# Performance work log

Hardware: AMD Instinct MI355X
Metric: run time of the kernel (lower is better)

The kernel has to match this reference:

```python
import jax, jax.numpy as jnp
import numpy as np

B, S, H = 32, 8192, 512


def setup_inputs() -> dict:
    key = jax.random.key(0)
    k1, k2, k3, k4 = jax.random.split(key, 4)
    output = jax.random.normal(k1, (B, 1, H), dtype=jnp.float32)
    context = jax.random.normal(k2, (B, S, H), dtype=jnp.float32)
    split_index = jax.random.randint(k3, (B,), 1, S - 1)  # avoid all-masked softmax rows
    W = jax.random.normal(k4, (H, 4 * H), dtype=jnp.float32) * (1.0 / np.sqrt(4 * H))
    b = jnp.zeros((H,), dtype=jnp.float32)
    return {"output": output, "context": context, "split_index": split_index, "W": W, "b": b}


def reference(output, context, split_index, W, b):
    Bb, Ss, Hh = context.shape
    rows = jnp.arange(Bb)
    pos = jnp.arange(Ss)

    # attn = bmm(output, context^T).squeeze(1) -> [B, S]
    attn = jnp.einsum('bih,bsh->bis', output, context)[:, 0, :]
    # torch code uses attn.data (detached) for all softmax paths
    attn_d = jax.lax.stop_gradient(attn)

    # forward-side mask: positions i < split_index kept
    fmask = pos[None, :] < split_index[:, None]  # [B, S] bool
    f_logits = jnp.where(fmask, attn_d, -jnp.inf)
    f_attn = jax.nn.softmax(f_logits, axis=1)
    f_attn = f_attn.at[rows, split_index].set(0.0)  # explicit zero at split position
    a_mix = jnp.einsum('bs,bsh->bh', f_attn, context)[:, None, :]  # [B,1,H]

    # NOTE: original source has `b_attn = f_attn.view(...)` (bug), so b_mix == a_mix.
    # The b-side masked softmax is computed but dead; we replicate the realized math.
    b_mix = a_mix

    # det_att = context[b, split_index[b], :]
    det_att = context[rows, split_index][:, None, :]  # [B,1,H]

    combined = jnp.concatenate((a_mix, b_mix, det_att, output), axis=2)  # [B,1,4H]
    out = jnp.tanh(combined @ W.T + b)  # Linear(4H->H) + Tanh, [B,1,H]
    return out, attn
```

## Files before the change

kernel.cpp:

```cpp
#include <hip/hip_runtime.h>
#include <math.h>

#define BATCH 32
#define SEQ   8192
#define HID   512
#define STRIPES 32
#define RPB   (SEQ / STRIPES)
#define CR    8
#define NCHUNK (RPB / CR)

typedef float f4 __attribute__((ext_vector_type(4)));
typedef float f2 __attribute__((ext_vector_type(2)));

#define VMWAIT(N) do { asm volatile("s_waitcnt vmcnt(" #N ")" ::: "memory"); \
                       __builtin_amdgcn_sched_barrier(0); } while (0)
#define LGKMWAIT0 do { asm volatile("s_waitcnt lgkmcnt(0)" ::: "memory"); \
                       __builtin_amdgcn_sched_barrier(0); } while (0)

__device__ __forceinline__ void gload_lds(const float* g, float* l) {
  __builtin_amdgcn_global_load_lds(
      (const __attribute__((address_space(1))) void*)g,
      (__attribute__((address_space(3))) void*)l, 16, 0, 0);
}

__global__ __launch_bounds__(256, 4) void k_pass1(
    const float* __restrict__ outp, const float* __restrict__ ctx,
    const int* __restrict__ split, float* __restrict__ attn_out,
    float* __restrict__ pacc, float* __restrict__ pmd)
{
  __shared__ float lds[2][CR][HID];
  const int tid = threadIdx.x, lane = tid & 63, wave = tid >> 6;
  const int b = blockIdx.x >> 5;
  const int stripe = blockIdx.x & 31;
  const int sp = split[b];
  const int s_base = stripe * RPB;

  const float* ob = outp + b * HID + lane * 8;
  const f4 o0 = *(const f4*)ob;
  const f4 o1 = *(const f4*)(ob + 4);

  const float* cbase = ctx + ((size_t)b * SEQ + s_base) * HID;
  float* ao = attn_out + (size_t)b * SEQ + s_base;

#pragma unroll
  for (int i = 0; i < 4; ++i) {
    const int o = (wave * 4 + i) * 256;
    gload_lds(cbase + o + lane * 4, &lds[0][0][0] + o);
  }
#pragma unroll
  for (int i = 0; i < 4; ++i) {
    const int o = (wave * 4 + i) * 256;
    gload_lds(cbase + CR * HID + o + lane * 4, &lds[1][0][0] + o);
  }

  float m = -INFINITY, d = 0.f;
  f4 acc0 = {0.f, 0.f, 0.f, 0.f}, acc1 = {0.f, 0.f, 0.f, 0.f};

#pragma unroll 1
  for (int c = 0; c < NCHUNK; ++c) {
    if (c == 0)                 VMWAIT(4);
    else if (c == NCHUNK - 1)   VMWAIT(1);
    else                        VMWAIT(5);

    const int cur = c & 1;
    f4 c0[2], c1[2];
#pragma unroll
    for (int k = 0; k < 2; ++k) {
      const float* rp = &lds[cur][wave * 2 + k][lane * 8];
      c0[k] = *(const f4*)rp;
      c1[k] = *(const f4*)(rp + 4);
    }
    LGKMWAIT0;

    float a2[2];
#pragma unroll
    for (int k = 0; k < 2; ++k) {
      float v = o0[0]*c0[k][0] + o0[1]*c0[k][1] + o0[2]*c0[k][2] + o0[3]*c0[k][3]
              + o1[0]*c1[k][0] + o1[1]*c1[k][1] + o1[2]*c1[k][2] + o1[3]*c1[k][3];
#pragma unroll
      for (int off = 32; off >= 1; off >>= 1) v += __shfl_xor(v, off, 64);
      a2[k] = v;
    }
    if (lane == 0) {
      f2 st = {a2[0], a2[1]};
      *(f2*)(ao + c * CR + wave * 2) = st;
    }

    if (c + 2 < NCHUNK) {
      const float* src = cbase + (size_t)(c + 2) * CR * HID;
      float* dst = &lds[cur][0][0];
#pragma unroll
      for (int i = 0; i < 4; ++i) {
        const int o = (wave * 4 + i) * 256;
        gload_lds(src + o + lane * 4, dst + o);
      }
    }

#pragma unroll
    for (int k = 0; k < 2; ++k) {
      const int s = s_base + c * CR + wave * 2 + k;
      if (s < sp) {
        const float v  = a2[k];
        const float nm = fmaxf(m, v);
        const float sc = __expf(m - nm);
        const float w  = __expf(v - nm);
        d = d * sc + w;
        acc0 = acc0 * sc + w * c0[k];
        acc1 = acc1 * sc + w * c1[k];
        m = nm;
      }
    }
  }

  __syncthreads();
  float* lacc = &lds[0][0][0];
  float* lmd  = &lds[1][0][0];
  *(f4*)(lacc + wave * HID + lane * 8)     = acc0;
  *(f4*)(lacc + wave * HID + lane * 8 + 4) = acc1;
  if (lane == 0) { lmd[wave * 2] = m; lmd[wave * 2 + 1] = d; }
  __syncthreads();

  const float M = fmaxf(fmaxf(lmd[0], lmd[2]), fmaxf(lmd[4], lmd[6]));
  const size_t pb = (size_t)b * STRIPES + stripe;
  float* pa = pacc + pb * HID;
  if (M == -INFINITY) {
    pa[tid * 2] = 0.f; pa[tid * 2 + 1] = 0.f;
    if (tid == 0) { pmd[pb * 2] = -INFINITY; pmd[pb * 2 + 1] = 0.f; }
  } else {
    float e[4], Dl = 0.f;
#pragma unroll
    for (int wv = 0; wv < 4; ++wv) {
      const float mw = lmd[wv * 2];
      e[wv] = (mw == -INFINITY) ? 0.f : __expf(mw - M);
      Dl += e[wv] * lmd[wv * 2 + 1];
    }
    float s0 = 0.f, s1 = 0.f;
#pragma unroll
    for (int wv = 0; wv < 4; ++wv) {
      s0 += e[wv] * lacc[wv * HID + tid * 2];
      s1 += e[wv] * lacc[wv * HID + tid * 2 + 1];
    }
    pa[tid * 2] = s0; pa[tid * 2 + 1] = s1;
    if (tid == 0) { pmd[pb * 2] = M; pmd[pb * 2 + 1] = Dl; }
  }
}

__global__ __launch_bounds__(256) void k_final(
    const float* __restrict__ outp, const float* __restrict__ ctx,
    const int* __restrict__ split, const float* __restrict__ W,
    const float* __restrict__ bias, const float* __restrict__ pacc,
    const float* __restrict__ pmd, float* __restrict__ out0)
{
  const int b = blockIdx.x >> 3, q = blockIdx.x & 7;
  const int tid = threadIdx.x;
  __shared__ float comb[3 * HID + 8];
  float* amixp = comb;
  float* detp  = comb + HID + 4;
  float* oupp  = comb + 2 * HID + 8;

  float M = -INFINITY;
#pragma unroll
  for (int c = 0; c < STRIPES; ++c) M = fmaxf(M, pmd[(b * STRIPES + c) * 2]);
  float wgt[STRIPES], D = 0.f;
#pragma unroll
  for (int c = 0; c < STRIPES; ++c) {
    const float mw = pmd[(b * STRIPES + c) * 2];
    wgt[c] = (mw == -INFINITY) ? 0.f : __expf(mw - M);
    D += wgt[c] * pmd[(b * STRIPES + c) * 2 + 1];
  }
  const float invD = 1.f / D;
  const int sp = split[b];
#pragma unroll
  for (int col = tid; col < HID; col += 256) {
    float s = 0.f;
#pragma unroll
    for (int c = 0; c < STRIPES; ++c)
      s += wgt[c] * pacc[((size_t)(b * STRIPES + c)) * HID + col];
    amixp[col] = s * invD;
    detp[col]  = ctx[((size_t)b * SEQ + sp) * HID + col];
    oupp[col]  = outp[b * HID + col];
  }
  __syncthreads();

  const int hl = tid >> 2, part = tid & 3;
  const int h = q * 64 + hl;
  const float* wr = W + (size_t)h * (4 * HID) + part * HID;
  const float* src = (part == 2) ? detp : (part == 3 ? oupp : amixp);
  float acc = 0.f;
#pragma unroll 4
  for (int k0 = 0; k0 < HID; k0 += 4) {
    const f4 w = *(const f4*)(wr + k0);
    const f4 x = *(const f4*)(src + k0);
    acc += w[0]*x[0] + w[1]*x[1] + w[2]*x[2] + w[3]*x[3];
  }
  acc += __shfl_xor(acc, 1, 64);
  acc += __shfl_xor(acc, 2, 64);
  if (part == 0) out0[b * HID + h] = tanhf(acc + bias[h]);
}

extern "C" void kernel_launch(void* const* d_in, const int* in_sizes, int n_in,
                              void* d_out, int out_size, void* d_ws, size_t ws_size,
                              hipStream_t stream)
{
  const float* outp = (const float*)d_in[0];
  const float* ctx  = (const float*)d_in[1];
  const int*   spl  = (const int*)d_in[2];
  const float* W    = (const float*)d_in[3];
  const float* bias = (const float*)d_in[4];

  float* out0   = (float*)d_out;
  float* attn_o = out0 + (size_t)BATCH * HID;

  float* pacc = (float*)d_ws;
  float* pmd  = pacc + (size_t)BATCH * STRIPES * HID;

  k_pass1<<<BATCH * STRIPES, 256, 0, stream>>>(outp, ctx, spl, attn_o, pacc, pmd);
  k_final<<<BATCH * 8,       256, 0, stream>>>(outp, ctx, spl, W, bias, pacc, pmd, out0);
}
```

Before: 126.0 us.

## Replace LDS double-buffered context staging with register prefetch pipeline per wave

Drops the global_load_lds double buffer with its manual waitcnt scheduling. Each wave now owns a contiguous run of 64 rows and streams them straight into registers with a software pipeline 4 row-pairs deep. Row data is also laid out so each lane reads two coalesced 16-byte segments. This removes the LDS round trip and the manual vmcnt bookkeeping, but raises register pressure (32 f4 in flight), which may limit occupancy under launch_bounds(256,4).

```diff
diff --git a/kernel.cpp b/kernel.cpp
--- a/kernel.cpp
+++ b/kernel.cpp
@@ -6,117 +6,113 @@
 #define HID   512
 #define STRIPES 32
 #define RPB   (SEQ / STRIPES)
-#define CR    8
-#define NCHUNK (RPB / CR)
+#define GPW   32
+#define DEPTH 4
 
 typedef float f4 __attribute__((ext_vector_type(4)));
 typedef float f2 __attribute__((ext_vector_type(2)));
-
-#define VMWAIT(N) do { asm volatile("s_waitcnt vmcnt(" #N ")" ::: "memory"); \
-                       __builtin_amdgcn_sched_barrier(0); } while (0)
-#define LGKMWAIT0 do { asm volatile("s_waitcnt lgkmcnt(0)" ::: "memory"); \
-                       __builtin_amdgcn_sched_barrier(0); } while (0)
-
-__device__ __forceinline__ void gload_lds(const float* g, float* l) {
-  __builtin_amdgcn_global_load_lds(
-      (const __attribute__((address_space(1))) void*)g,
-      (__attribute__((address_space(3))) void*)l, 16, 0, 0);
-}
 
 __global__ __launch_bounds__(256, 4) void k_pass1(
     const float* __restrict__ outp, const float* __restrict__ ctx,
     const int* __restrict__ split, float* __restrict__ attn_out,
     float* __restrict__ pacc, float* __restrict__ pmd)
 {
-  __shared__ float lds[2][CR][HID];
   const int tid = threadIdx.x, lane = tid & 63, wave = tid >> 6;
   const int b = blockIdx.x >> 5;
   const int stripe = blockIdx.x & 31;
   const int sp = split[b];
   const int s_base = stripe * RPB;
-
-  const float* ob = outp + b * HID + lane * 8;
-  const f4 o0 = *(const f4*)ob;
-  const f4 o1 = *(const f4*)(ob + 4);
-
-  const float* cbase = ctx + ((size_t)b * SEQ + s_base) * HID;
-  float* ao = attn_out + (size_t)b * SEQ + s_base;
-
-#pragma unroll
-  for (int i = 0; i < 4; ++i) {
-    const int o = (wave * 4 + i) * 256;
-    gload_lds(cbase + o + lane * 4, &lds[0][0][0] + o);
-  }
-#pragma unroll
-  for (int i = 0; i < 4; ++i) {
-    const int o = (wave * 4 + i) * 256;
-    gload_lds(cbase + CR * HID + o + lane * 4, &lds[1][0][0] + o);
+  const int w_base = s_base + wave * 64;
+
+  const float* ob = outp + b * HID;
+  const f4 o0 = *(const f4*)(ob + lane * 4);
+  const f4 o1 = *(const f4*)(ob + 256 + lane * 4);
+
+  const float* wb = ctx + ((size_t)b * SEQ + w_base) * HID;
+  float* ao = attn_out + (size_t)b * SEQ + w_base;
+
+  f4 r[DEPTH][2][2];
+#pragma unroll
+  for (int ji = 0; ji < DEPTH; ++ji) {
+    const float* gp = wb + (size_t)(2 * ji) * HID + lane * 4;
+    r[ji][0][0] = *(const f4*)gp;
+    r[ji][0][1] = *(const f4*)(gp + 256);
+    r[ji][1][0] = *(const f4*)(gp + HID);
+    r[ji][1][1] = *(const f4*)(gp + HID + 256);
   }
 
   float m = -INFINITY, d = 0.f;
   f4 acc0 = {0.f, 0.f, 0.f, 0.f}, acc1 = {0.f, 0.f, 0.f, 0.f};
 
+#define CONSUME(JIDX, C00, C01, C10, C11)                                      \
+  {                                                                            \
+    float a0, a1;                                                              \
+    {                                                                          \
+      float v = C00[0]*o0[0] + C00[1]*o0[1] + C00[2]*o0[2] + C00[3]*o0[3]      \
+              + C01[0]*o1[0] + C01[1]*o1[1] + C01[2]*o1[2] + C01[3]*o1[3];     \
+      _Pragma("unroll")                                                        \
+      for (int off = 32; off >= 1; off >>= 1) v += __shfl_xor(v, off, 64);     \
+      a0 = v;                                                                  \
+    }                                                                          \
+    {                                                                          \
+      float v = C10[0]*o0[0] + C10[1]*o0[1] + C10[2]*o0[2] + C10[3]*o0[3]      \
+              + C11[0]*o1[0] + C11[1]*o1[1] + C11[2]*o1[2] + C11[3]*o1[3];     \
+      _Pragma("unroll")                                                        \
+      for (int off = 32; off >= 1; off >>= 1) v += __shfl_xor(v, off, 64);     \
+      a1 = v;                                                                  \
+    }                                                                          \
+    if (lane == 0) { f2 st = {a0, a1}; *(f2*)(ao + 2 * (JIDX)) = st; }         \
+    {                                                                          \
+      const int s0 = w_base + 2 * (JIDX);                                      \
+      if (s0 < sp) {                                         \
+        const float nm = fmaxf(m, a0);                                         \
+        const float sc = __expf(m - nm);                                       \
+        const float w  = __expf(a0 - nm);                                      \
+        d = d * sc + w;                                                        \
+        acc0 = acc0 * sc + w * C00;                                            \
+        acc1 = acc1 * sc + w * C01;                                            \
+        m = nm;                                                                \
+      }                                                                        \
+      if (s0 + 1 < sp) {                                                       \
+        const float nm = fmaxf(m, a1);                                         \
+        const float sc = __expf(m - nm);                                       \
+        const float w  = __expf(a1 - nm);                                      \
+        d = d * sc + w;                                                        \
+        acc0 = acc0 * sc + w * C10;                                            \
+        acc1 = acc1 * sc + w * C11;                                            \
+        m = nm;                                                                \
+      }                                                                        \
+    }                                                                          \
+  }
+
 #pragma unroll 1
-  for (int c = 0; c < NCHUNK; ++c) {
-    if (c == 0)                 VMWAIT(4);
-    else if (c == NCHUNK - 1)   VMWAIT(1);
-    else                        VMWAIT(5);
-
-    const int cur = c & 1;
-    f4 c0[2], c1[2];
-#pragma unroll
-    for (int k = 0; k < 2; ++k) {
-      const float* rp = &lds[cur][wave * 2 + k][lane * 8];
-      c0[k] = *(const f4*)rp;
-      c1[k] = *(const f4*)(rp + 4);
+  for (int jo = 0; jo < GPW / DEPTH - 1; ++jo) {
+#pragma unroll
+    for (int ji = 0; ji < DEPTH; ++ji) {
+      const int j = jo * DEPTH + ji;
+      const f4 c00 = r[ji][0][0], c01 = r[ji][0][1];
+      const f4 c10 = r[ji][1][0], c11 = r[ji][1][1];
+      {
+        const float* gp = wb + (size_t)(2 * (j + DEPTH)) * HID + lane * 4;
+        r[ji][0][0] = *(const f4*)gp;
+        r[ji][0][1] = *(const f4*)(gp + 256);
+        r[ji][1][0] = *(const f4*)(gp + HID);
+        r[ji][1][1] = *(const f4*)(gp + HID + 256);
+      }
+      CONSUME(j, c00, c01, c10, c11);
     }
-    LGKMWAIT0;
-
-    float a2[2];
-#pragma unroll
-    for (int k = 0; k < 2; ++k) {
-      float v = o0[0]*c0[k][0] + o0[1]*c0[k][1] + o0[2]*c0[k][2] + o0[3]*c0[k][3]
-              + o1[0]*c1[k][0] + o1[1]*c1[k][1] + o1[2]*c1[k][2] + o1[3]*c1[k][3];
-#pragma unroll
-      for (int off = 32; off >= 1; off >>= 1) v += __shfl_xor(v, off, 64);
-      a2[k] = v;
-    }
-    if (lane == 0) {
-      f2 st = {a2[0], a2[1]};
-      *(f2*)(ao + c * CR + wave * 2) = st;
-    }
-
-    if (c + 2 < NCHUNK) {
-      const float* src = cbase + (size_t)(c + 2) * CR * HID;
-      float* dst = &lds[cur][0][0];
-#pragma unroll
-      for (int i = 0; i < 4; ++i) {
-        const int o = (wave * 4 + i) * 256;
-        gload_lds(src + o + lane * 4, dst + o);
-      }
-    }
-
-#pragma unroll
-    for (int k = 0; k < 2; ++k) {
-      const int s = s_base + c * CR + wave * 2 + k;
-      if (s < sp) {
-        const float v  = a2[k];
-        const float nm = fmaxf(m, v);
-        const float sc = __expf(m - nm);
-        const float w  = __expf(v - nm);
-        d = d * sc + w;
-        acc0 = acc0 * sc + w * c0[k];
-        acc1 = acc1 * sc + w * c1[k];
-        m = nm;
-      }
-    }
-  }
-
-  __syncthreads();
-  float* lacc = &lds[0][0][0];
-  float* lmd  = &lds[1][0][0];
-  *(f4*)(lacc + wave * HID + lane * 8)     = acc0;
-  *(f4*)(lacc + wave * HID + lane * 8 + 4) = acc1;
+  }
+#pragma unroll
+  for (int ji = 0; ji < DEPTH; ++ji) {
+    const int j = (GPW - DEPTH) + ji;
+    CONSUME(j, r[ji][0][0], r[ji][0][1], r[ji][1][0], r[ji][1][1]);
+  }
+#undef CONSUME
+
+  __shared__ float lacc[4 * HID];
+  __shared__ float lmd[8];
+  *(f4*)(lacc + wave * HID + lane * 4)       = acc0;
+  *(f4*)(lacc + wave * HID + 256 + lane * 4) = acc1;
   if (lane == 0) { lmd[wave * 2] = m; lmd[wave * 2 + 1] = d; }
   __syncthreads();
 
```

After: 147.7 us. +17.3%, slower.
